# Kernel tuning notes

Hardware: AMD Instinct MI355X
Metric: run time of the kernel (lower is better)

Reference implementation:

```python
import jax, jax.numpy as jnp
import numpy as np

# Config (Qwen3-4B-like, from ModelConfig defaults in source)
B = 32          # batch = number of decode requests = total_q
H = 32          # num_attention_heads
KVH = 8         # num_key_value_heads
G = H // KVH    # num_kv_groups = 4
D = 128         # head_dim
HID = 2560      # hidden_size
PS = 16         # page_size
MAXP = 128      # max_num_pages per request
NPAGES = B * MAXP   # 4096 pages in pool
MAXKV = MAXP * PS   # 2048
THETA = 5000000.0
EPS = 1e-6


def setup_inputs() -> dict:
    key = jax.random.key(0)
    ks = jax.random.split(key, 12)
    x = jax.random.normal(ks[0], (1, B, HID), dtype=jnp.float32)
    Wq = jax.random.normal(ks[1], (H * D, HID), dtype=jnp.float32) * 0.02
    Wk = jax.random.normal(ks[2], (KVH * D, HID), dtype=jnp.float32) * 0.02
    Wv = jax.random.normal(ks[3], (KVH * D, HID), dtype=jnp.float32) * 0.02
    Wo = jax.random.normal(ks[4], (HID, H * D), dtype=jnp.float32) * 0.02
    q_norm_w = jnp.ones((D,), dtype=jnp.float32)
    k_norm_w = jnp.ones((D,), dtype=jnp.float32)
    K_pool = jax.random.normal(ks[5], (NPAGES, PS, KVH, D), dtype=jnp.float32) * 0.02
    V_pool = jax.random.normal(ks[6], (NPAGES, PS, KVH, D), dtype=jnp.float32) * 0.02
    # each request owns a disjoint contiguous run of pages
    page_indices = jnp.arange(NPAGES, dtype=jnp.int32).reshape(B, MAXP)
    # KV length AFTER writing the single new decode token, in [128, MAXKV]
    lengths_after = jax.random.randint(ks[7], (B,), 128, MAXKV + 1).astype(jnp.int32)
    pos = lengths_after - 1                                  # position of new token
    page_of = page_indices[jnp.arange(B), pos // PS]         # page holding it
    slot_mapping = page_of.astype(jnp.int64) * PS + (pos % PS).astype(jnp.int64)
    # RoPE tables at the new-token positions: cos/sin (1, total_q, 1, D)
    inv_freq = 1.0 / (THETA ** (jnp.arange(0, D, 2, dtype=jnp.float32) / D))
    ang = pos.astype(jnp.float32)[:, None] * inv_freq[None, :]   # (B, D/2)
    ang = jnp.concatenate([ang, ang], axis=-1)                   # (B, D)
    cos = jnp.cos(ang)[None, :, None, :]
    sin = jnp.sin(ang)[None, :, None, :]
    return {"x": x, "cos": cos, "sin": sin, "Wq": Wq, "Wk": Wk, "Wv": Wv,
            "Wo": Wo, "q_norm_w": q_norm_w, "k_norm_w": k_norm_w,
            "K_pool": K_pool, "V_pool": V_pool, "page_indices": page_indices,
            "lengths_after": lengths_after, "slot_mapping": slot_mapping}


def _rmsnorm(x, w):
    xf = x.astype(jnp.float32)
    xf = xf * jax.lax.rsqrt(jnp.mean(xf * xf, axis=-1, keepdims=True) + EPS)
    return (w * xf).astype(x.dtype)


def _rope(x, cos, sin):
    # x: (1, heads, S, D); cos/sin: (1, S, 1, D) -> (1, 1, S, D)
    c = jnp.swapaxes(cos, 1, 2).astype(x.dtype)
    s = jnp.swapaxes(sin, 1, 2).astype(x.dtype)
    x1, x2 = jnp.split(x, 2, axis=-1)
    rot = jnp.concatenate([-x2, x1], axis=-1)
    return x * c + rot * s


def reference(x, cos, sin, Wq, Wk, Wv, Wo, q_norm_w, k_norm_w,
              K_pool, V_pool, page_indices, lengths_after, slot_mapping):
    total_q = x.shape[1]  # == B for decode
    # projections -> (1, heads, total_q, D)
    q = jnp.einsum('bsh,oh->bso', x, Wq).reshape(1, total_q, H, D).transpose(0, 2, 1, 3)
    k = jnp.einsum('bsh,oh->bso', x, Wk).reshape(1, total_q, KVH, D).transpose(0, 2, 1, 3)
    v = jnp.einsum('bsh,oh->bso', x, Wv).reshape(1, total_q, KVH, D).transpose(0, 2, 1, 3)
    # QK-norm (per-head RMSNorm on head_dim), then RoPE
    q = _rope(_rmsnorm(q, q_norm_w), cos, sin)
    k = _rope(_rmsnorm(k, k_norm_w), cos, sin)
    # write new K/V into the page pool (index_copy_ equivalent)
    k_pack = jnp.swapaxes(k[0], 0, 1)  # (total_q, KVH, D)
    v_pack = jnp.swapaxes(v[0], 0, 1)
    Kf = K_pool.reshape(NPAGES * PS, KVH, D).at[slot_mapping].set(k_pack)
    Vf = V_pool.reshape(NPAGES * PS, KVH, D).at[slot_mapping].set(v_pack)
    Kp = Kf.reshape(NPAGES, PS, KVH, D)
    Vp = Vf.reshape(NPAGES, PS, KVH, D)
    # decode path: full page-table gather per request
    flat_idx = page_indices.reshape(-1)
    k_all = Kp[flat_idx].reshape(B, MAXKV, KVH, D)
    v_all = Vp[flat_idx].reshape(B, MAXKV, KVH, D)
    # GQA attention, single query per request; scale = 1/sqrt(D) (SDPA default)
    qg = jnp.swapaxes(q[0], 0, 1).reshape(B, KVH, G, D)  # (B, KVH, G, D)
    scores = jnp.einsum('bkgd,bskd->bkgs', qg, k_all) * (1.0 / np.sqrt(D))
    invalid = jnp.arange(MAXKV)[None, :] >= lengths_after[:, None]  # (B, MAXKV)
    scores = jnp.where(invalid[:, None, None, :], -jnp.inf, scores)
    probs = jax.nn.softmax(scores, axis=-1)
    out = jnp.einsum('bkgs,bskd->bkgd', probs, v_all).reshape(B, H * D)
    y = jnp.einsum('bo,ho->bh', out, Wo)  # o_proj
    return y[None]  # (1, total_q, HID)
```

## Files before the change

kernel.cpp:

```cpp
#include <hip/hip_runtime.h>
#include <math.h>

#define NB    32
#define HIDV  2560
#define HD    128
#define NQH   32
#define NKVH  8

typedef __bf16 bf16x8 __attribute__((ext_vector_type(8)));
typedef float  f32x4  __attribute__((ext_vector_type(4)));

__device__ __forceinline__ unsigned bfpack(float a, float b) {
  unsigned ua = __float_as_uint(a), ub = __float_as_uint(b);
  ua = (ua + 0x7FFFu + ((ua >> 16) & 1u)) >> 16;
  ub = (ub + 0x7FFFu + ((ub >> 16) & 1u)) >> 16;
  return ua | (ub << 16);
}

__device__ __forceinline__ f32x4 nt_load4(const float* p) {
  return __builtin_nontemporal_load((const f32x4*)p);
}

__device__ __forceinline__ void gemm_body(
    const float* __restrict__ X, const float* __restrict__ W,
    float* __restrict__ P, int N, int K, int f0, int kc0, int slabs, int t,
    unsigned short* Wl, unsigned short* Xl) {
  const int w = t >> 6, l = t & 63;
  const int rA = l & 15, kq = l >> 4;
  f32x4 acc0 = {0.f, 0.f, 0.f, 0.f}, acc1 = {0.f, 0.f, 0.f, 0.f};

  for (int s = 0; s < slabs; ++s) {
    const int kc = kc0 * slabs + s;
    if (s) __syncthreads();
    const float* Wg = W + (size_t)f0 * K + (size_t)kc * 256;
    #pragma unroll
    for (int i = 0; i < 16; ++i) {
      int idx = i * 256 + t;
      int row = idx >> 6, c4 = idx & 63;
      f32x4 w4 = nt_load4(Wg + (size_t)row * K + c4 * 4);
      *(uint2*)((char*)Wl + row * 528 + c4 * 8) =
          make_uint2(bfpack(w4.x, w4.y), bfpack(w4.z, w4.w));
    }
    const float* Xg = X + (size_t)kc * 256;
    #pragma unroll
    for (int i = 0; i < 8; ++i) {
      int idx = i * 256 + t;
      int row = idx >> 6, c4 = idx & 63;
      float4 x4 = *(const float4*)(Xg + (size_t)row * K + c4 * 4);
      *(uint2*)((char*)Xl + row * 528 + c4 * 8) =
          make_uint2(bfpack(x4.x, x4.y), bfpack(x4.z, x4.w));
    }
    __syncthreads();

    const char* pa0 = (const char*)Xl + rA * 528 + kq * 16;
    const char* pa1 = pa0 + 16 * 528;
    const char* pb  = (const char*)Wl + (w * 16 + rA) * 528 + kq * 16;
    #pragma unroll
    for (int ks = 0; ks < 8; ++ks) {
      bf16x8 a0 = *(const bf16x8*)(pa0 + ks * 64);
      bf16x8 a1 = *(const bf16x8*)(pa1 + ks * 64);
      bf16x8 bb = *(const bf16x8*)(pb  + ks * 64);
      acc0 = __builtin_amdgcn_mfma_f32_16x16x32_bf16(a0, bb, acc0, 0, 0, 0);
      acc1 = __builtin_amdgcn_mfma_f32_16x16x32_bf16(a1, bb, acc1, 0, 0, 0);
    }
  }
  const int fcol = f0 + w * 16 + rA;
  float* Pr = P + ((size_t)kc0 * 32) * N + fcol;
  #pragma unroll
  for (int j = 0; j < 4; ++j) {
    int b0 = kq * 4 + j;
    Pr[(size_t)b0 * N]        = acc0[j];
    Pr[(size_t)(b0 + 16) * N] = acc1[j];
  }
}

__global__ __launch_bounds__(256) void qkv_gemm(
    const float* __restrict__ X, const float* __restrict__ Wq,
    const float* __restrict__ Wk, const float* __restrict__ Wv,
    float* __restrict__ qp, float* __restrict__ kp, float* __restrict__ vp) {
  __shared__ __align__(16) unsigned short Wl[64 * 264];
  __shared__ __align__(16) unsigned short Xl[32 * 264];
  const int bx = blockIdx.x;
  const float* W; float* P; int N, f0;
  if (bx < 64)      { W = Wq; P = qp; N = 4096; f0 = bx * 64; }
  else if (bx < 80) { W = Wk; P = kp; N = 1024; f0 = (bx - 64) * 64; }
  else              { W = Wv; P = vp; N = 1024; f0 = (bx - 80) * 64; }
  gemm_body(X, W, P, N, 2560, f0, blockIdx.y, 2, threadIdx.x, Wl, Xl);
}

__global__ __launch_bounds__(256) void o_gemm(
    const float* __restrict__ X, const float* __restrict__ W,
    float* __restrict__ P) {
  __shared__ __align__(16) unsigned short Wl[64 * 264];
  __shared__ __align__(16) unsigned short Xl[32 * 264];
  gemm_body(X, W, P, 2560, 4096, blockIdx.x * 64, blockIdx.y, 2, threadIdx.x, Wl, Xl);
}

__global__ __launch_bounds__(512) void attn(
    const float* __restrict__ Kp, const float* __restrict__ Vp,
    const float* __restrict__ qp, const float* __restrict__ kp,
    const float* __restrict__ vp, const float* __restrict__ cosb,
    const float* __restrict__ sinb, const float* __restrict__ qw,
    const float* __restrict__ kw, const int* __restrict__ pidx,
    const int* __restrict__ lens, float* __restrict__ ao) {
  const int b = blockIdx.x >> 3, kvh = blockIdx.x & 7;
  const int t = threadIdx.x, w = t >> 6, l = t & 63;
  const int sub = l >> 4, di = (l & 15) * 8;
  __shared__ int pages[128];
  __shared__ float mmS[32][4], msS[32][4];
  __shared__ __align__(16) float maccS[32][4][128];
  float* qlds = &maccS[0][0][0];
  float* klds = qlds + 512;
  float* vlds = klds + 128;
  float* rsum = vlds + 128;

  if (t < 128) pages[t] = pidx[b * 128 + t];

  const int role = t >> 7, d = t & 127;
  float xq = 0.f;
  #pragma unroll
  for (int c = 0; c < 5; ++c)
    xq += qp[((size_t)c * 32 + b) * 4096 + (kvh * 4 + role) * 128 + d];
  float xk = 0.f, xv = 0.f;
  if (t < 128) {
    #pragma unroll
    for (int c = 0; c < 5; ++c)
      xk += kp[((size_t)c * 32 + b) * 1024 + kvh * 128 + d];
  } else if (t < 256) {
    #pragma unroll
    for (int c = 0; c < 5; ++c)
      xv += vp[((size_t)c * 32 + b) * 1024 + kvh * 128 + d];
  }
  float ssq = xq * xq;
  #pragma unroll
  for (int mk = 1; mk < 64; mk <<= 1) ssq += __shfl_xor(ssq, mk);
  if (l == 0) rsum[w] = ssq;
  if (t < 128) {
    float ssk = xk * xk;
    #pragma unroll
    for (int mk = 1; mk < 64; mk <<= 1) ssk += __shfl_xor(ssk, mk);
    if (l == 0) rsum[8 + w] = ssk;
  }
  __syncthreads();
  const float cb = cosb[b * 128 + d], sb = sinb[b * 128 + d];
  const float invq = rsqrtf((rsum[role * 2] + rsum[role * 2 + 1]) * (1.f / 128.f) + 1e-6f);
  const float xnq = xq * invq * qw[d];
  qlds[role * 128 + d] = xnq;
  float xnk = 0.f;
  if (t < 128) {
    const float invk = rsqrtf((rsum[8] + rsum[9]) * (1.f / 128.f) + 1e-6f);
    xnk = xk * invk * kw[d];
    klds[d] = xnk;
  } else if (t < 256) {
    vlds[d] = xv;
  }
  __syncthreads();
  const float rpq = qlds[role * 128 + (d ^ 64)];
  const float rpk = (t < 128) ? klds[d ^ 64] : 0.f;
  __syncthreads();
  qlds[role * 128 + d] = xnq * cb + ((d < 64) ? -rpq : rpq) * sb;
  if (t < 128) klds[d] = xnk * cb + ((d < 64) ? -rpk : rpk) * sb;
  __syncthreads();

  const int len = lens[b], lim = len - 1;
  float qf[4][8];
  const float SC = 0.08838834764831845f * 1.4426950408889634f;
  #pragma unroll
  for (int g = 0; g < 4; ++g)
    #pragma unroll
    for (int j = 0; j < 8; ++j)
      qf[g][j] = qlds[g * 128 + di + j] * SC;

  float m[4], se[4], acc[4][8];
  #pragma unroll
  for (int g = 0; g < 4; ++g) {
    m[g] = -INFINITY; se[g] = 0.f;
    #pragma unroll
    for (int j = 0; j < 8; ++j) acc[g][j] = 0.f;
  }

  const int t0 = w * 4 + sub;
  const int nit = (lim + 31) >> 5;
  f32x4 k0, k1, v0, v1;
  {
    int tt = min(t0, lim - 1);
    size_t a = ((size_t)pages[tt >> 4] * 16 + (tt & 15)) * 1024 + kvh * 128 + di;
    k0 = nt_load4(Kp + a); k1 = nt_load4(Kp + a + 4);
    v0 = nt_load4(Vp + a); v1 = nt_load4(Vp + a + 4);
  }
  for (int it = 0; it < nit; ++it) {
    const float ck[8] = {k0[0], k0[1], k0[2], k0[3], k1[0], k1[1], k1[2], k1[3]};
    const float cv[8] = {v0[0], v0[1], v0[2], v0[3], v1[0], v1[1], v1[2], v1[3]};
    const bool valid = it * 32 + t0 < lim;
    if (it + 1 < nit) {
      int tt = min((it + 1) * 32 + t0, lim - 1);
      size_t a = ((size_t)pages[tt >> 4] * 16 + (tt & 15)) * 1024 + kvh * 128 + di;
      k0 = nt_load4(Kp + a); k1 = nt_load4(Kp + a + 4);
      v0 = nt_load4(Vp + a); v1 = nt_load4(Vp + a + 4);
    }
    float s[4];
    #pragma unroll
    for (int g = 0; g < 4; ++g) {
      float d8 = 0.f;
      #pragma unroll
      for (int j = 0; j < 8; ++j) d8 += qf[g][j] * ck[j];
      s[g] = d8;
    }
    #pragma unroll
    for (int mk = 1; mk < 16; mk <<= 1) {
      #pragma unroll
      for (int g = 0; g < 4; ++g) s[g] += __shfl_xor(s[g], mk);
    }
    if (valid) {
      #pragma unroll
      for (int g = 0; g < 4; ++g) {
        const float sg = s[g];
        if (sg > m[g]) {
          const float scf = exp2f(m[g] - sg);
          m[g] = sg;
          se[g] = se[g] * scf + 1.f;
          #pragma unroll
          for (int j = 0; j < 8; ++j) acc[g][j] = acc[g][j] * scf + cv[j];
        } else {
          const float p = exp2f(sg - m[g]);
          se[g] += p;
          #pragma unroll
          for (int j = 0; j < 8; ++j) acc[g][j] += p * cv[j];
        }
      }
    }
  }

  if (w == 0) {
    float ck[8], cv[8];
    #pragma unroll
    for (int j = 0; j < 8; ++j) { ck[j] = klds[di + j]; cv[j] = vlds[di + j]; }
    float s[4];
    #pragma unroll
    for (int g = 0; g < 4; ++g) {
      float d8 = 0.f;
      #pragma unroll
      for (int j = 0; j < 8; ++j) d8 += qf[g][j] * ck[j];
      s[g] = d8;
    }
    #pragma unroll
    for (int mk = 1; mk < 16; mk <<= 1) {
      #pragma unroll
      for (int g = 0; g < 4; ++g) s[g] += __shfl_xor(s[g], mk);
    }
    if (sub == 0) {
      #pragma unroll
      for (int g = 0; g < 4; ++g) {
        const float sg = s[g];
        if (sg > m[g]) {
          const float scf = exp2f(m[g] - sg);
          m[g] = sg;
          se[g] = se[g] * scf + 1.f;
          #pragma unroll
          for (int j = 0; j < 8; ++j) acc[g][j] = acc[g][j] * scf + cv[j];
        } else {
          const float p = exp2f(sg - m[g]);
          se[g] += p;
          #pragma unroll
          for (int j = 0; j < 8; ++j) acc[g][j] += p * cv[j];
        }
      }
    }
  }

  const int st = w * 4 + sub;
  if ((l & 15) == 0) {
    #pragma unroll
    for (int g = 0; g < 4; ++g) { mmS[st][g] = m[g]; msS[st][g] = se[g]; }
  }
  #pragma unroll
  for (int g = 0; g < 4; ++g)
    #pragma unroll
    for (int j = 0; j < 8; ++j) maccS[st][g][di + j] = acc[g][j];
  __syncthreads();

  const int g = t >> 7, dd = t & 127;
  float M = -INFINITY;
  #pragma unroll
  for (int s2 = 0; s2 < 32; ++s2) M = fmaxf(M, mmS[s2][g]);
  float den = 0.f, num = 0.f;
  for (int s2 = 0; s2 < 32; ++s2) {
    const float wg = exp2f(mmS[s2][g] - M);
    den += wg * msS[s2][g];
    num += wg * maccS[s2][g][dd];
  }
  ao[((size_t)b * 32 + kvh * 4 + g) * 128 + dd] = num / den;
}

__global__ __launch_bounds__(256) void oreduce(const float* __restrict__ op,
                                               float* __restrict__ y) {
  const int i = blockIdx.x * 256 + threadIdx.x;
  float s = 0.f;
  #pragma unroll
  for (int c = 0; c < 8; ++c) s += op[(size_t)c * (32 * 2560) + i];
  y[i] = s;
}

extern "C" void kernel_launch(void* const* d_in, const int* in_sizes, int n_in,
                              void* d_out, int out_size, void* d_ws, size_t ws_size,
                              hipStream_t stream) {
  const float* x    = (const float*)d_in[0];
  const float* cosb = (const float*)d_in[1];
  const float* sinb = (const float*)d_in[2];
  const float* Wq   = (const float*)d_in[3];
  const float* Wk   = (const float*)d_in[4];
  const float* Wv   = (const float*)d_in[5];
  const float* Wo   = (const float*)d_in[6];
  const float* qw   = (const float*)d_in[7];
  const float* kw   = (const float*)d_in[8];
  const float* Kp   = (const float*)d_in[9];
  const float* Vp   = (const float*)d_in[10];
  const int*   pidx = (const int*)d_in[11];
  const int*   lens = (const int*)d_in[12];
  float* y = (float*)d_out;

  float* ws = (float*)d_ws;
  float* qp = ws;
  float* kp = qp + 655360;
  float* vp = kp + 163840;
  float* ao = vp + 163840;
  float* op = qp;
  (void)in_sizes; (void)n_in; (void)out_size; (void)ws_size;

  qkv_gemm<<<dim3(96, 5), 256, 0, stream>>>(x, Wq, Wk, Wv, qp, kp, vp);
  attn<<<256, 512, 0, stream>>>(Kp, Vp, qp, kp, vp, cosb, sinb, qw, kw, pidx, lens, ao);
  o_gemm<<<dim3(40, 8), 256, 0, stream>>>(ao, Wo, op);
  oreduce<<<320, 256, 0, stream>>>(op, y);
}
```

Measured before the change: 111.6 us.

## Fuse split-K o-proj reduction via atomics, double-buffer attention KV loads

The o_proj kernel now accumulates its split-K partials straight into the output with atomicAdd after a memset, which removes the separate reduction kernel and the partial buffer round-trip. Nontemporal loads are replaced with ordinary loads in both the GEMM and the attention kernel. The attention loop is unrolled by two, keeping two independent K/V prefetch sets in flight, and the per-token update is factored into a lambda. The atomics make the summation order nondeterministic, and the memset adds a small operation to the stream.

```diff
diff --git a/kernel.cpp b/kernel.cpp
--- a/kernel.cpp
+++ b/kernel.cpp
@@ -15,10 +15,6 @@
   ua = (ua + 0x7FFFu + ((ua >> 16) & 1u)) >> 16;
   ub = (ub + 0x7FFFu + ((ub >> 16) & 1u)) >> 16;
   return ua | (ub << 16);
-}
-
-__device__ __forceinline__ f32x4 nt_load4(const float* p) {
-  return __builtin_nontemporal_load((const f32x4*)p);
 }
 
 __device__ __forceinline__ void gemm_body(
@@ -37,7 +33,7 @@
     for (int i = 0; i < 16; ++i) {
       int idx = i * 256 + t;
       int row = idx >> 6, c4 = idx & 63;
-      f32x4 w4 = nt_load4(Wg + (size_t)row * K + c4 * 4);
+      float4 w4 = *(const float4*)(Wg + (size_t)row * K + c4 * 4);
       *(uint2*)((char*)Wl + row * 528 + c4 * 8) =
           make_uint2(bfpack(w4.x, w4.y), bfpack(w4.z, w4.w));
     }
@@ -88,15 +84,63 @@
   gemm_body(X, W, P, N, 2560, f0, blockIdx.y, 2, threadIdx.x, Wl, Xl);
 }
 
-__global__ __launch_bounds__(256) void o_gemm(
+__global__ __launch_bounds__(256) void o_gemm_a(
     const float* __restrict__ X, const float* __restrict__ W,
-    float* __restrict__ P) {
+    float* __restrict__ y) {
   __shared__ __align__(16) unsigned short Wl[64 * 264];
   __shared__ __align__(16) unsigned short Xl[32 * 264];
-  gemm_body(X, W, P, 2560, 4096, blockIdx.x * 64, blockIdx.y, 2, threadIdx.x, Wl, Xl);
-}
-
-__global__ __launch_bounds__(512) void attn(
+  const int t = threadIdx.x;
+  const int K = 4096, f0 = blockIdx.x * 64, kc0 = blockIdx.y;
+  const int w = t >> 6, l = t & 63;
+  const int rA = l & 15, kq = l >> 4;
+  f32x4 acc0 = {0.f, 0.f, 0.f, 0.f}, acc1 = {0.f, 0.f, 0.f, 0.f};
+
+  for (int s = 0; s < 2; ++s) {
+    const int kc = kc0 * 2 + s;
+    if (s) __syncthreads();
+    const float* Wg = W + (size_t)f0 * K + (size_t)kc * 256;
+    #pragma unroll
+    for (int i = 0; i < 16; ++i) {
+      int idx = i * 256 + t;
+      int row = idx >> 6, c4 = idx & 63;
+      float4 w4 = *(const float4*)(Wg + (size_t)row * K + c4 * 4);
+      *(uint2*)((char*)Wl + row * 528 + c4 * 8) =
+          make_uint2(bfpack(w4.x, w4.y), bfpack(w4.z, w4.w));
+    }
+    const float* Xg = X + (size_t)kc * 256;
+    #pragma unroll
+    for (int i = 0; i < 8; ++i) {
+      int idx = i * 256 + t;
+      int row = idx >> 6, c4 = idx & 63;
+      float4 x4 = *(const float4*)(Xg + (size_t)row * K + c4 * 4);
+      *(uint2*)((char*)Xl + row * 528 + c4 * 8) =
+          make_uint2(bfpack(x4.x, x4.y), bfpack(x4.z, x4.w));
+    }
+    __syncthreads();
+
+    const char* pa0 = (const char*)Xl + rA * 528 + kq * 16;
+    const char* pa1 = pa0 + 16 * 528;
+    const char* pb  = (const char*)Wl + (w * 16 + rA) * 528 + kq * 16;
+    #pragma unroll
+    for (int ks = 0; ks < 8; ++ks) {
+      bf16x8 a0 = *(const bf16x8*)(pa0 + ks * 64);
+      bf16x8 a1 = *(const bf16x8*)(pa1 + ks * 64);
+      bf16x8 bb = *(const bf16x8*)(pb  + ks * 64);
+      acc0 = __builtin_amdgcn_mfma_f32_16x16x32_bf16(a0, bb, acc0, 0, 0, 0);
+      acc1 = __builtin_amdgcn_mfma_f32_16x16x32_bf16(a1, bb, acc1, 0, 0, 0);
+    }
+  }
+  const int fcol = f0 + w * 16 + rA;
+  float* Yr = y + fcol;
+  #pragma unroll
+  for (int j = 0; j < 4; ++j) {
+    int b0 = kq * 4 + j;
+    atomicAdd(&Yr[(size_t)b0 * 2560],        acc0[j]);
+    atomicAdd(&Yr[(size_t)(b0 + 16) * 2560], acc1[j]);
+  }
+}
+
+__global__ __launch_bounds__(512) void attn_f(
     const float* __restrict__ Kp, const float* __restrict__ Vp,
     const float* __restrict__ qp, const float* __restrict__ kp,
     const float* __restrict__ vp, const float* __restrict__ cosb,
@@ -170,6 +214,7 @@
     #pragma unroll
     for (int j = 0; j < 8; ++j)
       qf[g][j] = qlds[g * 128 + di + j] * SC;
+  __syncthreads();
 
   float m[4], se[4], acc[4][8];
   #pragma unroll
@@ -181,23 +226,8 @@
 
   const int t0 = w * 4 + sub;
   const int nit = (lim + 31) >> 5;
-  f32x4 k0, k1, v0, v1;
-  {
-    int tt = min(t0, lim - 1);
-    size_t a = ((size_t)pages[tt >> 4] * 16 + (tt & 15)) * 1024 + kvh * 128 + di;
-    k0 = nt_load4(Kp + a); k1 = nt_load4(Kp + a + 4);
-    v0 = nt_load4(Vp + a); v1 = nt_load4(Vp + a + 4);
-  }
-  for (int it = 0; it < nit; ++it) {
-    const float ck[8] = {k0[0], k0[1], k0[2], k0[3], k1[0], k1[1], k1[2], k1[3]};
-    const float cv[8] = {v0[0], v0[1], v0[2], v0[3], v1[0], v1[1], v1[2], v1[3]};
-    const bool valid = it * 32 + t0 < lim;
-    if (it + 1 < nit) {
-      int tt = min((it + 1) * 32 + t0, lim - 1);
-      size_t a = ((size_t)pages[tt >> 4] * 16 + (tt & 15)) * 1024 + kvh * 128 + di;
-      k0 = nt_load4(Kp + a); k1 = nt_load4(Kp + a + 4);
-      v0 = nt_load4(Vp + a); v1 = nt_load4(Vp + a + 4);
-    }
+
+  auto update = [&](const float (&ck)[8], const float (&cv)[8], bool valid) {
     float s[4];
     #pragma unroll
     for (int g = 0; g < 4; ++g) {
@@ -229,43 +259,51 @@
         }
       }
     }
+  };
+
+  f32x4 ka0, ka1, va0, va1, kb0, kb1, vb0, vb1;
+  {
+    int tt = min(t0, lim - 1);
+    size_t a = ((size_t)pages[tt >> 4] * 16 + (tt & 15)) * 1024 + kvh * 128 + di;
+    ka0 = *(const f32x4*)(Kp + a); ka1 = *(const f32x4*)(Kp + a + 4);
+    va0 = *(const f32x4*)(Vp + a); va1 = *(const f32x4*)(Vp + a + 4);
+  }
+  if (nit > 1) {
+    int tt = min(32 + t0, lim - 1);
+    size_t a = ((size_t)pages[tt >> 4] * 16 + (tt & 15)) * 1024 + kvh * 128 + di;
+    kb0 = *(const f32x4*)(Kp + a); kb1 = *(const f32x4*)(Kp + a + 4);
+    vb0 = *(const f32x4*)(Vp + a); vb1 = *(const f32x4*)(Vp + a + 4);
+  }
+  for (int it = 0; it < nit; it += 2) {
+    {
+      const float ck[8] = {ka0[0], ka0[1], ka0[2], ka0[3], ka1[0], ka1[1], ka1[2], ka1[3]};
+      const float cv[8] = {va0[0], va0[1], va0[2], va0[3], va1[0], va1[1], va1[2], va1[3]};
+      if (it + 2 < nit) {
+        int tt = min((it + 2) * 32 + t0, lim - 1);
+        size_t a = ((size_t)pages[tt >> 4] * 16 + (tt & 15)) * 1024 + kvh * 128 + di;
+        ka0 = *(const f32x4*)(Kp + a); ka1 = *(const f32x4*)(Kp + a + 4);
+        va0 = *(const f32x4*)(Vp + a); va1 = *(const f32x4*)(Vp + a + 4);
+      }
+      update(ck, cv, it * 32 + t0 < lim);
+    }
+    if (it + 1 < nit) {
+      const float ck[8] = {kb0[0], kb0[1], kb0[2], kb0[3], kb1[0], kb1[1], kb1[2], kb1[3]};
+      const float cv[8] = {vb0[0], vb0[1], vb0[2], vb0[3], vb1[0], vb1[1], vb1[2], vb1[3]};
+      if (it + 3 < nit) {
+        int tt = min((it + 3) * 32 + t0, lim - 1);
+        size_t a = ((size_t)pages[tt >> 4] * 16 + (tt & 15)) * 1024 + kvh * 128 + di;
+        kb0 = *(const f32x4*)(Kp + a); kb1 = *(const f32x4*)(Kp + a + 4);
+        vb0 = *(const f32x4*)(Vp + a); vb1 = *(const f32x4*)(Vp + a + 4);
+      }
+      update(ck, cv, (it + 1) * 32 + t0 < lim);
+    }
   }
 
   if (w == 0) {
     float ck[8], cv[8];
     #pragma unroll
     for (int j = 0; j < 8; ++j) { ck[j] = klds[di + j]; cv[j] = vlds[di + j]; }
-    float s[4];
-    #pragma unroll
-    for (int g = 0; g < 4; ++g) {
-      float d8 = 0.f;
-      #pragma unroll
-      for (int j = 0; j < 8; ++j) d8 += qf[g][j] * ck[j];
-      s[g] = d8;
-    }
-    #pragma unroll
-    for (int mk = 1; mk < 16; mk <<= 1) {
-      #pragma unroll
-      for (int g = 0; g < 4; ++g) s[g] += __shfl_xor(s[g], mk);
-    }
-    if (sub == 0) {
-      #pragma unroll
-      for (int g = 0; g < 4; ++g) {
-        const float sg = s[g];
-        if (sg > m[g]) {
-          const float scf = exp2f(m[g] - sg);
-          m[g] = sg;
-          se[g] = se[g] * scf + 1.f;
-          #pragma unroll
-          for (int j = 0; j < 8; ++j) acc[g][j] = acc[g][j] * scf + cv[j];
-        } else {
-          const float p = exp2f(sg - m[g]);
-          se[g] += p;
-          #pragma unroll
-          for (int j = 0; j < 8; ++j) acc[g][j] += p * cv[j];
-        }
-      }
-    }
+    update(ck, cv, sub == 0);
   }
 
   const int st = w * 4 + sub;
@@ -290,15 +328,6 @@
     num += wg * maccS[s2][g][dd];
   }
   ao[((size_t)b * 32 + kvh * 4 + g) * 128 + dd] = num / den;
-}
-
-__global__ __launch_bounds__(256) void oreduce(const float* __restrict__ op,
-                                               float* __restrict__ y) {
-  const int i = blockIdx.x * 256 + threadIdx.x;
-  float s = 0.f;
-  #pragma unroll
-  for (int c = 0; c < 8; ++c) s += op[(size_t)c * (32 * 2560) + i];
-  y[i] = s;
 }
 
 extern "C" void kernel_launch(void* const* d_in, const int* in_sizes, int n_in,
@@ -324,11 +353,11 @@
   float* kp = qp + 655360;
   float* vp = kp + 163840;
   float* ao = vp + 163840;
-  float* op = qp;
   (void)in_sizes; (void)n_in; (void)out_size; (void)ws_size;
 
+  hipMemsetAsync(y, 0, (size_t)32 * 2560 * sizeof(float), stream);
   qkv_gemm<<<dim3(96, 5), 256, 0, stream>>>(x, Wq, Wk, Wv, qp, kp, vp);
-  attn<<<256, 512, 0, stream>>>(Kp, Vp, qp, kp, vp, cosb, sinb, qw, kw, pidx, lens, ao);
-  o_gemm<<<dim3(40, 8), 256, 0, stream>>>(ao, Wo, op);
-  oreduce<<<320, 256, 0, stream>>>(op, y);
-}
+  attn_f<<<256, 512, 0, stream>>>(Kp, Vp, qp, kp, vp, cosb, sinb, qw, kw,
+                                  pidx, lens, ao);
+  o_gemm_a<<<dim3(40, 8), 256, 0, stream>>>(ao, Wo, y);
+}
```

After: 99.28 us. 1.12x faster.
